# Optimization experiments

Measured on AMD Instinct MI355X. Metric: run time of the kernel, lower is better.

The kernel has to match this reference:

```python
import jax, jax.numpy as jnp
import numpy as np
import math

B, S, D_MODEL, H, D_K = 8, 1024, 512, 8, 64


def setup_inputs() -> dict:
    key = jax.random.key(0)
    ks = jax.random.split(key, 12)
    s = 1.0 / math.sqrt(D_MODEL)
    inp = {
        "q": jax.random.normal(ks[0], (B, S, D_MODEL), dtype=jnp.float32),
        "k": jax.random.normal(ks[1], (B, S, D_MODEL), dtype=jnp.float32),
        "v": jax.random.normal(ks[2], (B, S, D_MODEL), dtype=jnp.float32),
        "Wq": jax.random.normal(ks[3], (D_MODEL, D_MODEL), dtype=jnp.float32) * s,
        "bq": jnp.zeros((D_MODEL,), dtype=jnp.float32),
        "Wk": jax.random.normal(ks[4], (D_MODEL, D_MODEL), dtype=jnp.float32) * s,
        "bk": jnp.zeros((D_MODEL,), dtype=jnp.float32),
        "Wv": jax.random.normal(ks[5], (D_MODEL, D_MODEL), dtype=jnp.float32) * s,
        "bv": jnp.zeros((D_MODEL,), dtype=jnp.float32),
        "Wo": jax.random.normal(ks[6], (D_MODEL, D_MODEL), dtype=jnp.float32) * s,
        "bo": jnp.zeros((D_MODEL,), dtype=jnp.float32),
        # xavier_uniform on (H,1,1): bound = sqrt(6/(1+1)) ~ 1.732
        "gammas": jax.random.uniform(ks[7], (H, 1, 1), minval=-1.732, maxval=1.732, dtype=jnp.float32),
        "mask": jnp.triu(jnp.ones((S, S), dtype=bool), k=1),  # mask future positions
        "key_padding_mask": jnp.zeros((B, S), dtype=bool),
    }
    return inp


def reference(q, k, v, Wq, bq, Wk, bk, Wv, bv, Wo, bo, gammas, mask, key_padding_mask):
    bs, seqlen = q.shape[0], q.shape[1]
    NEG = -1e32

    def proj(x, W, b):
        # nn.Linear: x @ W.T + b, then split heads -> [b, h, s, d_k]
        return (x @ W.T + b).reshape(bs, seqlen, H, D_K).transpose(0, 2, 1, 3)

    qh, kh, vh = proj(q, Wq, bq), proj(k, Wk, bk), proj(v, Wv, bv)

    scores = jnp.einsum("bhqd,bhkd->bhqk", qh, kh) / math.sqrt(D_K)
    full_mask = mask[None, None, :, :] | key_padding_mask[:, None, None, :]  # [b,1,s,s] bcast over h

    # --- distance-decay branch (torch.no_grad / detach) ---
    scores_ = jax.nn.softmax(jnp.where(full_mask, NEG, scores), axis=-1)
    scores_ = scores_ * (~full_mask).astype(scores.dtype)
    distcum = jnp.cumsum(scores_, axis=-1)  # forward=True
    disttotal = jnp.sum(scores_, axis=-1, keepdims=True)
    idx = jnp.arange(seqlen)
    position_effect = jnp.abs(idx[None, :] - idx[:, None]).astype(scores.dtype)  # |i-j|
    dist_scores = jnp.sqrt(jnp.clip((disttotal - distcum) * position_effect, 0.0))
    dist_scores = jax.lax.stop_gradient(dist_scores)

    gamma = -jax.nn.softplus(gammas)[None]  # [1, h, 1, 1]
    total_effect = jnp.clip(jnp.exp(dist_scores * gamma), 1e-5, 1e5)

    attn = jax.nn.softmax(jnp.where(full_mask, NEG, scores * total_effect), axis=-1)
    out = jnp.einsum("bhqk,bhkd->bhqd", attn, vh)
    concat = out.transpose(0, 2, 1, 3).reshape(bs, seqlen, D_MODEL)
    return concat @ Wo.T + bo
```

## Files before the change

kernel.cpp:

```cpp
#include <hip/hip_runtime.h>
#include <hip/hip_bf16.h>
#include <math.h>

#define NB   8
#define NS   1024
#define NDM  512
#define NH   8
#define NDK  64
#define NM   8192

typedef __attribute__((ext_vector_type(8))) short short8;
typedef __attribute__((ext_vector_type(4))) float f32x4;

__device__ __forceinline__ unsigned short f2b(float f) {
    __hip_bfloat16 h = __float2bfloat16(f);
    unsigned short u;
    __builtin_memcpy(&u, &h, 2);
    return u;
}
__device__ __forceinline__ float b2f(unsigned short u) {
    return __uint_as_float(((unsigned)u) << 16);
}
__device__ __forceinline__ float exp2_raw(float x) { float r; asm("v_exp_f32 %0, %1" : "=v"(r) : "v"(x)); return r; }
__device__ __forceinline__ float sqrt_raw(float x) { float r; asm("v_sqrt_f32 %0, %1" : "=v"(r) : "v"(x)); return r; }
__device__ __forceinline__ float rcp_raw(float x)  { float r; asm("v_rcp_f32 %0, %1" : "=v"(r) : "v"(x)); return r; }

template<int CTRL, int RM>
__device__ __forceinline__ float dpp_mov0(float x) {
    int m = __builtin_amdgcn_update_dpp(0, __float_as_int(x), CTRL, RM, 0xf, true);
    return __int_as_float(m);
}
__device__ __forceinline__ float wave_incl_scan(float x) {
    x += dpp_mov0<0x111, 0xf>(x);
    x += dpp_mov0<0x112, 0xf>(x);
    x += dpp_mov0<0x114, 0xf>(x);
    x += dpp_mov0<0x118, 0xf>(x);
    x += dpp_mov0<0x142, 0xa>(x);
    x += dpp_mov0<0x143, 0xc>(x);
    return x;
}
__device__ __forceinline__ float lane63(float x) {
    return __int_as_float(__builtin_amdgcn_readlane(__float_as_int(x), 63));
}

__device__ __forceinline__ short8 pack8(float4 a, float4 b) {
    short8 r;
    r[0] = (short)f2b(a.x); r[1] = (short)f2b(a.y);
    r[2] = (short)f2b(a.z); r[3] = (short)f2b(a.w);
    r[4] = (short)f2b(b.x); r[5] = (short)f2b(b.y);
    r[6] = (short)f2b(b.z); r[7] = (short)f2b(b.w);
    return r;
}

template<int OMODE, bool ACVT>
__device__ __forceinline__ void gemm_body(unsigned short* As, unsigned short* Bs,
                                          const void* __restrict__ Ap,
                                          const float* __restrict__ Wf,
                                          const float* __restrict__ bias,
                                          void* __restrict__ outp) {
    const int tid  = threadIdx.x;
    const int lane = tid & 63;
    const int wid  = tid >> 6;
    const int l15  = lane & 15, lhi = lane >> 4;
    const int m0 = (blockIdx.x >> 2) * 128;
    const int n0 = (blockIdx.x & 3) * 128;
    const int wr = wid >> 1, wc = wid & 1;

    const float* Af = (const float*)Ap;
    const unsigned short* Ab = (const unsigned short*)Ap;

    f32x4 acc[4][4];
#pragma unroll
    for (int i = 0; i < 4; ++i)
#pragma unroll
        for (int j = 0; j < 4; ++j) acc[i][j] = (f32x4){0.f, 0.f, 0.f, 0.f};

    for (int kk0 = 0; kk0 < NDM; kk0 += 32) {
#pragma unroll
        for (int c = 0; c < 2; ++c) {
            int ci  = tid + 256 * c;
            int row = ci >> 2;
            int kc  = (ci & 3) << 3;
            short8 aval;
            if (ACVT) {
                const float* p = Af + (size_t)(m0 + row) * NDM + kk0 + kc;
                aval = pack8(*(const float4*)p, *(const float4*)(p + 4));
            } else {
                aval = *(const short8*)(Ab + (size_t)(m0 + row) * NDM + kk0 + kc);
            }
            *(short8*)(As + ci * 8) = aval;
            const float* qp = Wf + (size_t)(n0 + row) * NDM + kk0 + kc;
            *(short8*)(Bs + ci * 8) = pack8(*(const float4*)qp, *(const float4*)(qp + 4));
        }
        __syncthreads();
        short8 af[4], bf[4];
#pragma unroll
        for (int mi = 0; mi < 4; ++mi)
            af[mi] = *(const short8*)(As + (wr * 64 + mi * 16 + l15) * 32 + lhi * 8);
#pragma unroll
        for (int ni = 0; ni < 4; ++ni)
            bf[ni] = *(const short8*)(Bs + (wc * 64 + ni * 16 + l15) * 32 + lhi * 8);
#pragma unroll
        for (int mi = 0; mi < 4; ++mi)
#pragma unroll
            for (int ni = 0; ni < 4; ++ni)
                acc[mi][ni] = __builtin_amdgcn_mfma_f32_16x16x32_bf16(af[mi], bf[ni], acc[mi][ni], 0, 0, 0);
        __syncthreads();
    }

#pragma unroll
    for (int mi = 0; mi < 4; ++mi) {
#pragma unroll
        for (int ni = 0; ni < 4; ++ni) {
            int row0 = m0 + wr * 64 + mi * 16 + lhi * 4;
            int col  = n0 + wc * 64 + ni * 16 + l15;
            float bv = bias[col];
            if (OMODE == 0) {
                unsigned short* o = (unsigned short*)outp;
                int h = col >> 6, d = col & 63;
#pragma unroll
                for (int r = 0; r < 4; ++r) {
                    int m = row0 + r;
                    int b = m >> 10, s = m & 1023;
                    o[(size_t)(((b * NH + h) * NS) + s) * NDK + d] = f2b(acc[mi][ni][r] + bv);
                }
            } else if (OMODE == 1) {
                unsigned short* o = (unsigned short*)outp;
                int h = col >> 6, d = col & 63;
                int b = row0 >> 10, s0 = row0 & 1023;
                ushort4 u;
                u.x = f2b(acc[mi][ni][0] + bv);
                u.y = f2b(acc[mi][ni][1] + bv);
                u.z = f2b(acc[mi][ni][2] + bv);
                u.w = f2b(acc[mi][ni][3] + bv);
                *(ushort4*)(o + (size_t)((b * NH + h) * NDK + d) * NS + s0) = u;
            } else {
                float* o = (float*)outp;
#pragma unroll
                for (int r = 0; r < 4; ++r)
                    o[(size_t)(row0 + r) * NDM + col] = acc[mi][ni][r] + bv;
            }
        }
    }
}

__global__ __launch_bounds__(256) void qkv_gemm(const float* __restrict__ q,
                                                const float* __restrict__ k,
                                                const float* __restrict__ v,
                                                const float* __restrict__ Wq,
                                                const float* __restrict__ Wk,
                                                const float* __restrict__ Wv,
                                                const float* __restrict__ bq,
                                                const float* __restrict__ bk,
                                                const float* __restrict__ bv,
                                                unsigned short* __restrict__ Qh,
                                                unsigned short* __restrict__ Kh,
                                                unsigned short* __restrict__ Vt) {
    __shared__ unsigned short As[128 * 32];
    __shared__ unsigned short Bs[128 * 32];
    const int y = blockIdx.y;
    if (y == 0)      gemm_body<0, true>(As, Bs, q, Wq, bq, Qh);
    else if (y == 1) gemm_body<0, true>(As, Bs, k, Wk, bk, Kh);
    else             gemm_body<1, true>(As, Bs, v, Wv, bv, Vt);
}

__global__ __launch_bounds__(256) void wo_gemm(const unsigned short* __restrict__ A,
                                               const float* __restrict__ Wo,
                                               const float* __restrict__ bo,
                                               float* __restrict__ out) {
    __shared__ unsigned short As[128 * 32];
    __shared__ unsigned short Bs[128 * 32];
    gemm_body<2, false>(As, Bs, A, Wo, bo, out);
}

__global__ __launch_bounds__(256, 4) void attn_kernel(const unsigned short* __restrict__ Qh,
                                                      const unsigned short* __restrict__ Kh,
                                                      const unsigned short* __restrict__ Vt,
                                                      const float* __restrict__ gammas,
                                                      unsigned short* __restrict__ concat) {
    __shared__ unsigned short pb[16 * 1024];
    const int bh   = blockIdx.x & 63;
    const int pair = blockIdx.x >> 6;
    const int tid = threadIdx.x, lane = tid & 63, wid = tid >> 6;
    const int l15 = lane & 15, lhi = lane >> 4;
    const float SC = 0.125f * 1.44269504f;

    const unsigned short* Kb = Kh + (size_t)bh * NS * NDK;
    const unsigned short* Vb = Vt + (size_t)bh * NDK * NS;
    const float g  = gammas[bh & (NH - 1)];
    const float g2 = -log1pf(__expf(g)) * 1.44269504f;
    const int cb = lane * 16;
    const int bq_ = bh >> 3, hq = bh & 7;

    for (int hs = 0; hs < 2; ++hs) {
        const int qt = hs ? (63 - pair) : pair;
        const int r0 = qt * 16;
        const int C  = ((r0 + 16 + 63) >> 6) << 6;

        const unsigned short* Qb = Qh + (size_t)(bh * NS + r0) * NDK;
        short8 qf0 = *(const short8*)(Qb + l15 * NDK + lhi * 8);
        short8 qf1 = *(const short8*)(Qb + l15 * NDK + lhi * 8 + 32);
        for (int j0 = wid * 16; j0 < C; j0 += 64) {
            const unsigned short* kp = Kb + (size_t)(j0 + l15) * NDK + lhi * 8;
            short8 kf0 = *(const short8*)kp;
            short8 kf1 = *(const short8*)(kp + 32);
            f32x4 a = {0.f, 0.f, 0.f, 0.f};
            a = __builtin_amdgcn_mfma_f32_16x16x32_bf16(kf0, qf0, a, 0, 0, 0);
            a = __builtin_amdgcn_mfma_f32_16x16x32_bf16(kf1, qf1, a, 0, 0, 0);
            ushort4 u;
            u.x = f2b(a[0] * SC);
            u.y = f2b(a[1] * SC);
            u.z = f2b(a[2] * SC);
            u.w = f2b(a[3] * SC);
            int ch = ((j0 >> 3) + (lhi >> 1)) ^ l15;
            *(ushort4*)(pb + l15 * 1024 + ch * 8 + (lhi & 1) * 4) = u;
        }
        __syncthreads();

#pragma unroll
        for (int t = 0; t < 4; ++t) {
            const int rr = wid + 4 * t;
            const int i  = r0 + rr;
            unsigned short* rowp = pb + rr * 1024;
            short8 raw0 = *(const short8*)(rowp + (((2 * lane)     ^ rr) << 3));
            short8 raw1 = *(const short8*)(rowp + (((2 * lane + 1) ^ rr) << 3));
            float s[16];
#pragma unroll
            for (int u = 0; u < 8; ++u) {
                s[u]     = b2f((unsigned short)raw0[u]);
                s[8 + u] = b2f((unsigned short)raw1[u]);
            }
#pragma unroll
            for (int u = 0; u < 16; ++u)
                if (cb + u > i) s[u] = -1e30f;
            float p[16];
            float run = 0.f;
#pragma unroll
            for (int u = 0; u < 16; ++u) { run += exp2_raw(s[u]); p[u] = run; }
            const float inc      = wave_incl_scan(run);
            const float l1       = lane63(inc);
            const float invl1    = rcp_raw(l1);
            const float taillane = l1 - (inc - run);
            const float di       = (float)(i - cb);
            float l2 = 0.f;
#pragma unroll
            for (int u = 0; u < 16; ++u) {
                float tail = fmaxf(taillane - p[u], 0.f);
                float t2   = (tail * invl1) * (di - (float)u);
                float te   = fmaxf(exp2_raw(g2 * sqrt_raw(t2)), 1e-5f);
                float w    = exp2_raw(s[u] * te);
                s[u] = w;
                l2 += w;
            }
            const float l2t  = lane63(wave_incl_scan(l2));
            const float inv2 = rcp_raw(l2t);
            short8 h0, h1;
#pragma unroll
            for (int u = 0; u < 8; ++u) {
                h0[u] = (short)f2b(s[u] * inv2);
                h1[u] = (short)f2b(s[8 + u] * inv2);
            }
            *(short8*)(rowp + (((2 * lane)     ^ rr) << 3)) = h0;
            *(short8*)(rowp + (((2 * lane + 1) ^ rr) << 3)) = h1;
        }
        __syncthreads();

        const int d0 = wid * 16;
        f32x4 acc = {0.f, 0.f, 0.f, 0.f};
        for (int j0 = 0; j0 < C; j0 += 32) {
            short8 av = *(const short8*)(Vb + (size_t)(d0 + l15) * NS + j0 + lhi * 8);
            short8 pw = *(const short8*)(pb + l15 * 1024 + (((((j0 >> 3) + lhi)) ^ l15) << 3));
            acc = __builtin_amdgcn_mfma_f32_16x16x32_bf16(av, pw, acc, 0, 0, 0);
        }
        {
            int d = d0 + lhi * 4;
            int s = r0 + l15;
            ushort4 u;
            u.x = f2b(acc[0]); u.y = f2b(acc[1]);
            u.z = f2b(acc[2]); u.w = f2b(acc[3]);
            *(ushort4*)(concat + (size_t)(bq_ * NS + s) * NDM + hq * NDK + d) = u;
        }
        __syncthreads();
    }
}

extern "C" void kernel_launch(void* const* d_in, const int* in_sizes, int n_in,
                              void* d_out, int out_size, void* d_ws, size_t ws_size,
                              hipStream_t stream) {
    const float* q  = (const float*)d_in[0];
    const float* k  = (const float*)d_in[1];
    const float* v  = (const float*)d_in[2];
    const float* Wq = (const float*)d_in[3];
    const float* bq = (const float*)d_in[4];
    const float* Wk = (const float*)d_in[5];
    const float* bk = (const float*)d_in[6];
    const float* Wv = (const float*)d_in[7];
    const float* bv = (const float*)d_in[8];
    const float* Wo = (const float*)d_in[9];
    const float* bo = (const float*)d_in[10];
    const float* gm = (const float*)d_in[11];

    char* w = (char*)d_ws;
    unsigned short* Qh     = (unsigned short*)(w);
    unsigned short* Kh     = (unsigned short*)(w + (size_t)8388608);
    unsigned short* Vt     = (unsigned short*)(w + (size_t)16777216);
    unsigned short* concat = (unsigned short*)(w + (size_t)25165824);

    qkv_gemm<<<dim3(256, 3), dim3(256), 0, stream>>>(q, k, v, Wq, Wk, Wv, bq, bk, bv, Qh, Kh, Vt);
    attn_kernel<<<dim3(2048), dim3(256), 0, stream>>>(Qh, Kh, Vt, gm, concat);
    wo_gemm<<<dim3(256), dim3(256), 0, stream>>>(concat, Wo, bo, (float*)d_out);
}
```

Baseline: 135.7 us.

## Pre-convert QKV weights, retile GEMMs to 64x128 with swizzled LDS, halve attention row tiles

Adds a pre-pass that converts Wq/Wk/Wv to bf16 once, using the output buffer as scratch, so the QKV GEMM can stream B tiles with global_load_lds instead of converting fp32 inside every block. Both GEMMs move to 64x128 tiles with a K-step of 64 and an XOR-swizzled LDS layout, which doubles the grid and raises occupancy hints. The attention kernel splits each 16-row query tile into two 8-row halves across separate blocks, halving LDS use and doubling the block count for better occupancy. In exchange, half of each score MFMA's output and the final PV tile is discarded, so matrix-core work per useful row roughly doubles, and there is one extra launch.

```diff
diff --git a/kernel.cpp b/kernel.cpp
--- a/kernel.cpp
+++ b/kernel.cpp
@@ -52,67 +52,101 @@
     return r;
 }
 
-template<int OMODE, bool ACVT>
-__device__ __forceinline__ void gemm_body(unsigned short* As, unsigned short* Bs,
-                                          const void* __restrict__ Ap,
-                                          const float* __restrict__ Wf,
-                                          const float* __restrict__ bias,
-                                          void* __restrict__ outp) {
-    const int tid  = threadIdx.x;
-    const int lane = tid & 63;
-    const int wid  = tid >> 6;
-    const int l15  = lane & 15, lhi = lane >> 4;
-    const int m0 = (blockIdx.x >> 2) * 128;
+__device__ __forceinline__ void gload16(const unsigned short* g, unsigned short* l) {
+    __builtin_amdgcn_global_load_lds(
+        (const __attribute__((address_space(1))) void*)g,
+        (__attribute__((address_space(3))) void*)l, 16, 0, 0);
+}
+
+__global__ __launch_bounds__(256) void cvt_w3(const float* __restrict__ Wq,
+                                              const float* __restrict__ Wk,
+                                              const float* __restrict__ Wv,
+                                              unsigned short* __restrict__ out) {
+    int idx = blockIdx.x * 256 + threadIdx.x;
+    int m = idx >> 16;
+    const float* s = (m == 0) ? Wq : ((m == 1) ? Wk : Wv);
+    float4 f = *(const float4*)(s + (size_t)(idx & 65535) * 4);
+    ushort4 u;
+    u.x = f2b(f.x); u.y = f2b(f.y); u.z = f2b(f.z); u.w = f2b(f.w);
+    *(ushort4*)(out + (size_t)idx * 4) = u;
+}
+
+template<int OMODE, bool ACVT, bool BCVT>
+__device__ __forceinline__ void gemm_body64(unsigned short* As, unsigned short* Bs,
+                                            const void* __restrict__ Ap,
+                                            const void* __restrict__ Wp,
+                                            const float* __restrict__ bias,
+                                            void* __restrict__ outp) {
+    const int tid = threadIdx.x, lane = tid & 63, wid = tid >> 6;
+    const int l15 = lane & 15, lhi = lane >> 4;
+    const int m0 = (blockIdx.x >> 2) * 64;
     const int n0 = (blockIdx.x & 3) * 128;
     const int wr = wid >> 1, wc = wid & 1;
-
     const float* Af = (const float*)Ap;
     const unsigned short* Ab = (const unsigned short*)Ap;
-
-    f32x4 acc[4][4];
-#pragma unroll
-    for (int i = 0; i < 4; ++i)
+    const float* Wf = (const float*)Wp;
+    const unsigned short* Wb = (const unsigned short*)Wp;
+
+    f32x4 acc[2][4];
+#pragma unroll
+    for (int i = 0; i < 2; ++i)
 #pragma unroll
         for (int j = 0; j < 4; ++j) acc[i][j] = (f32x4){0.f, 0.f, 0.f, 0.f};
 
-    for (int kk0 = 0; kk0 < NDM; kk0 += 32) {
+    for (int kk0 = 0; kk0 < NDM; kk0 += 64) {
 #pragma unroll
         for (int c = 0; c < 2; ++c) {
-            int ci  = tid + 256 * c;
-            int row = ci >> 2;
-            int kc  = (ci & 3) << 3;
-            short8 aval;
+            int ci = tid + 256 * c, row = ci >> 3, ch = ci & 7;
+            int sch = ch ^ (row & 7);
             if (ACVT) {
-                const float* p = Af + (size_t)(m0 + row) * NDM + kk0 + kc;
-                aval = pack8(*(const float4*)p, *(const float4*)(p + 4));
+                const float* p = Af + (size_t)(m0 + row) * NDM + kk0 + ch * 8;
+                *(short8*)(As + row * 64 + sch * 8) = pack8(*(const float4*)p, *(const float4*)(p + 4));
             } else {
-                aval = *(const short8*)(Ab + (size_t)(m0 + row) * NDM + kk0 + kc);
-            }
-            *(short8*)(As + ci * 8) = aval;
-            const float* qp = Wf + (size_t)(n0 + row) * NDM + kk0 + kc;
-            *(short8*)(Bs + ci * 8) = pack8(*(const float4*)qp, *(const float4*)(qp + 4));
-        }
-        __syncthreads();
-        short8 af[4], bf[4];
-#pragma unroll
-        for (int mi = 0; mi < 4; ++mi)
-            af[mi] = *(const short8*)(As + (wr * 64 + mi * 16 + l15) * 32 + lhi * 8);
+                gload16(Ab + (size_t)(m0 + row) * NDM + kk0 + sch * 8, As + ci * 8);
+            }
+        }
+#pragma unroll
+        for (int c = 0; c < 4; ++c) {
+            int ci = tid + 256 * c, row = ci >> 3, ch = ci & 7;
+            int sch = ch ^ (row & 7);
+            if (BCVT) {
+                const float* p = Wf + (size_t)(n0 + row) * NDM + kk0 + ch * 8;
+                *(short8*)(Bs + row * 64 + sch * 8) = pack8(*(const float4*)p, *(const float4*)(p + 4));
+            } else {
+                gload16(Wb + (size_t)(n0 + row) * NDM + kk0 + sch * 8, Bs + ci * 8);
+            }
+        }
+        __syncthreads();
+        short8 af[2][2], bf[4][2];
+#pragma unroll
+        for (int mi = 0; mi < 2; ++mi)
+#pragma unroll
+            for (int kk = 0; kk < 2; ++kk) {
+                int row = wr * 32 + mi * 16 + l15;
+                af[mi][kk] = *(const short8*)(As + row * 64 + (((kk * 4 + lhi) ^ (l15 & 7)) << 3));
+            }
 #pragma unroll
         for (int ni = 0; ni < 4; ++ni)
-            bf[ni] = *(const short8*)(Bs + (wc * 64 + ni * 16 + l15) * 32 + lhi * 8);
-#pragma unroll
-        for (int mi = 0; mi < 4; ++mi)
-#pragma unroll
-            for (int ni = 0; ni < 4; ++ni)
-                acc[mi][ni] = __builtin_amdgcn_mfma_f32_16x16x32_bf16(af[mi], bf[ni], acc[mi][ni], 0, 0, 0);
+#pragma unroll
+            for (int kk = 0; kk < 2; ++kk) {
+                int row = wc * 64 + ni * 16 + l15;
+                bf[ni][kk] = *(const short8*)(Bs + row * 64 + (((kk * 4 + lhi) ^ (l15 & 7)) << 3));
+            }
+#pragma unroll
+        for (int mi = 0; mi < 2; ++mi)
+#pragma unroll
+            for (int ni = 0; ni < 4; ++ni) {
+                acc[mi][ni] = __builtin_amdgcn_mfma_f32_16x16x32_bf16(af[mi][0], bf[ni][0], acc[mi][ni], 0, 0, 0);
+                acc[mi][ni] = __builtin_amdgcn_mfma_f32_16x16x32_bf16(af[mi][1], bf[ni][1], acc[mi][ni], 0, 0, 0);
+            }
         __syncthreads();
     }
 
 #pragma unroll
-    for (int mi = 0; mi < 4; ++mi) {
+    for (int mi = 0; mi < 2; ++mi) {
 #pragma unroll
         for (int ni = 0; ni < 4; ++ni) {
-            int row0 = m0 + wr * 64 + mi * 16 + lhi * 4;
+            int row0 = m0 + wr * 32 + mi * 16 + lhi * 4;
             int col  = n0 + wc * 64 + ni * 16 + l15;
             float bv = bias[col];
             if (OMODE == 0) {
@@ -144,43 +178,45 @@
     }
 }
 
-__global__ __launch_bounds__(256) void qkv_gemm(const float* __restrict__ q,
-                                                const float* __restrict__ k,
-                                                const float* __restrict__ v,
-                                                const float* __restrict__ Wq,
-                                                const float* __restrict__ Wk,
-                                                const float* __restrict__ Wv,
-                                                const float* __restrict__ bq,
-                                                const float* __restrict__ bk,
-                                                const float* __restrict__ bv,
-                                                unsigned short* __restrict__ Qh,
-                                                unsigned short* __restrict__ Kh,
-                                                unsigned short* __restrict__ Vt) {
-    __shared__ unsigned short As[128 * 32];
-    __shared__ unsigned short Bs[128 * 32];
+__global__ __launch_bounds__(256, 4) void qkv_gemm(const float* __restrict__ q,
+                                                   const float* __restrict__ k,
+                                                   const float* __restrict__ v,
+                                                   const unsigned short* __restrict__ Wqb,
+                                                   const unsigned short* __restrict__ Wkb,
+                                                   const unsigned short* __restrict__ Wvb,
+                                                   const float* __restrict__ bq,
+                                                   const float* __restrict__ bk,
+                                                   const float* __restrict__ bv,
+                                                   unsigned short* __restrict__ Qh,
+                                                   unsigned short* __restrict__ Kh,
+                                                   unsigned short* __restrict__ Vt) {
+    __shared__ unsigned short As[64 * 64];
+    __shared__ unsigned short Bs[128 * 64];
     const int y = blockIdx.y;
-    if (y == 0)      gemm_body<0, true>(As, Bs, q, Wq, bq, Qh);
-    else if (y == 1) gemm_body<0, true>(As, Bs, k, Wk, bk, Kh);
-    else             gemm_body<1, true>(As, Bs, v, Wv, bv, Vt);
-}
-
-__global__ __launch_bounds__(256) void wo_gemm(const unsigned short* __restrict__ A,
-                                               const float* __restrict__ Wo,
-                                               const float* __restrict__ bo,
-                                               float* __restrict__ out) {
-    __shared__ unsigned short As[128 * 32];
-    __shared__ unsigned short Bs[128 * 32];
-    gemm_body<2, false>(As, Bs, A, Wo, bo, out);
-}
-
-__global__ __launch_bounds__(256, 4) void attn_kernel(const unsigned short* __restrict__ Qh,
+    if (y == 0)      gemm_body64<0, true, false>(As, Bs, q, Wqb, bq, Qh);
+    else if (y == 1) gemm_body64<0, true, false>(As, Bs, k, Wkb, bk, Kh);
+    else             gemm_body64<1, true, false>(As, Bs, v, Wvb, bv, Vt);
+}
+
+__global__ __launch_bounds__(256, 4) void wo_gemm(const unsigned short* __restrict__ A,
+                                                  const float* __restrict__ Wo,
+                                                  const float* __restrict__ bo,
+                                                  float* __restrict__ out) {
+    __shared__ unsigned short As[64 * 64];
+    __shared__ unsigned short Bs[128 * 64];
+    gemm_body64<2, false, true>(As, Bs, A, Wo, bo, out);
+}
+
+__global__ __launch_bounds__(256, 8) void attn_kernel(const unsigned short* __restrict__ Qh,
                                                       const unsigned short* __restrict__ Kh,
                                                       const unsigned short* __restrict__ Vt,
                                                       const float* __restrict__ gammas,
                                                       unsigned short* __restrict__ concat) {
-    __shared__ unsigned short pb[16 * 1024];
+    __shared__ unsigned short pb[8 * 1024];
     const int bh   = blockIdx.x & 63;
-    const int pair = blockIdx.x >> 6;
+    const int ph   = blockIdx.x >> 6;
+    const int half = ph & 1;
+    const int pair = ph >> 1;
     const int tid = threadIdx.x, lane = tid & 63, wid = tid >> 6;
     const int l15 = lane & 15, lhi = lane >> 4;
     const float SC = 0.125f * 1.44269504f;
@@ -193,11 +229,11 @@
     const int bq_ = bh >> 3, hq = bh & 7;
 
     for (int hs = 0; hs < 2; ++hs) {
-        const int qt = hs ? (63 - pair) : pair;
-        const int r0 = qt * 16;
-        const int C  = ((r0 + 16 + 63) >> 6) << 6;
-
-        const unsigned short* Qb = Qh + (size_t)(bh * NS + r0) * NDK;
+        const int qt  = hs ? (63 - pair) : pair;
+        const int r0h = qt * 16 + half * 8;
+        const int C   = ((r0h + 8 + 63) >> 6) << 6;
+
+        const unsigned short* Qb = Qh + (size_t)(bh * NS + qt * 16) * NDK;
         short8 qf0 = *(const short8*)(Qb + l15 * NDK + lhi * 8);
         short8 qf1 = *(const short8*)(Qb + l15 * NDK + lhi * 8 + 32);
         for (int j0 = wid * 16; j0 < C; j0 += 64) {
@@ -207,23 +243,26 @@
             f32x4 a = {0.f, 0.f, 0.f, 0.f};
             a = __builtin_amdgcn_mfma_f32_16x16x32_bf16(kf0, qf0, a, 0, 0, 0);
             a = __builtin_amdgcn_mfma_f32_16x16x32_bf16(kf1, qf1, a, 0, 0, 0);
-            ushort4 u;
-            u.x = f2b(a[0] * SC);
-            u.y = f2b(a[1] * SC);
-            u.z = f2b(a[2] * SC);
-            u.w = f2b(a[3] * SC);
-            int ch = ((j0 >> 3) + (lhi >> 1)) ^ l15;
-            *(ushort4*)(pb + l15 * 1024 + ch * 8 + (lhi & 1) * 4) = u;
-        }
-        __syncthreads();
-
-#pragma unroll
-        for (int t = 0; t < 4; ++t) {
-            const int rr = wid + 4 * t;
-            const int i  = r0 + rr;
-            unsigned short* rowp = pb + rr * 1024;
-            short8 raw0 = *(const short8*)(rowp + (((2 * lane)     ^ rr) << 3));
-            short8 raw1 = *(const short8*)(rowp + (((2 * lane + 1) ^ rr) << 3));
+            if ((l15 >> 3) == half) {
+                int rowl = l15 & 7;
+                ushort4 u;
+                u.x = f2b(a[0] * SC);
+                u.y = f2b(a[1] * SC);
+                u.z = f2b(a[2] * SC);
+                u.w = f2b(a[3] * SC);
+                int ch = (((j0 >> 3) + (lhi >> 1)) ^ rowl);
+                *(ushort4*)(pb + rowl * 1024 + ch * 8 + (lhi & 1) * 4) = u;
+            }
+        }
+        __syncthreads();
+
+#pragma unroll
+        for (int t = 0; t < 2; ++t) {
+            const int rrl = wid + 4 * t;
+            const int i   = r0h + rrl;
+            unsigned short* rowp = pb + rrl * 1024;
+            short8 raw0 = *(const short8*)(rowp + (((2 * lane)     ^ rrl) << 3));
+            short8 raw1 = *(const short8*)(rowp + (((2 * lane + 1) ^ rrl) << 3));
             float s[16];
 #pragma unroll
             for (int u = 0; u < 8; ++u) {
@@ -260,8 +299,8 @@
                 h0[u] = (short)f2b(s[u] * inv2);
                 h1[u] = (short)f2b(s[8 + u] * inv2);
             }
-            *(short8*)(rowp + (((2 * lane)     ^ rr) << 3)) = h0;
-            *(short8*)(rowp + (((2 * lane + 1) ^ rr) << 3)) = h1;
+            *(short8*)(rowp + (((2 * lane)     ^ rrl) << 3)) = h0;
+            *(short8*)(rowp + (((2 * lane + 1) ^ rrl) << 3)) = h1;
         }
         __syncthreads();
 
@@ -269,12 +308,13 @@
         f32x4 acc = {0.f, 0.f, 0.f, 0.f};
         for (int j0 = 0; j0 < C; j0 += 32) {
             short8 av = *(const short8*)(Vb + (size_t)(d0 + l15) * NS + j0 + lhi * 8);
-            short8 pw = *(const short8*)(pb + l15 * 1024 + (((((j0 >> 3) + lhi)) ^ l15) << 3));
+            int rowl = l15 & 7;
+            short8 pw = *(const short8*)(pb + rowl * 1024 + (((((j0 >> 3) + lhi)) ^ rowl) << 3));
             acc = __builtin_amdgcn_mfma_f32_16x16x32_bf16(av, pw, acc, 0, 0, 0);
         }
-        {
+        if (l15 < 8) {
             int d = d0 + lhi * 4;
-            int s = r0 + l15;
+            int s = r0h + l15;
             ushort4 u;
             u.x = f2b(acc[0]); u.y = f2b(acc[1]);
             u.z = f2b(acc[2]); u.w = f2b(acc[3]);
@@ -306,7 +346,12 @@
     unsigned short* Vt     = (unsigned short*)(w + (size_t)16777216);
     unsigned short* concat = (unsigned short*)(w + (size_t)25165824);
 
-    qkv_gemm<<<dim3(256, 3), dim3(256), 0, stream>>>(q, k, v, Wq, Wk, Wv, bq, bk, bv, Qh, Kh, Vt);
-    attn_kernel<<<dim3(2048), dim3(256), 0, stream>>>(Qh, Kh, Vt, gm, concat);
-    wo_gemm<<<dim3(256), dim3(256), 0, stream>>>(concat, Wo, bo, (float*)d_out);
-}
+    unsigned short* Wqb = (unsigned short*)d_out;
+    unsigned short* Wkb = Wqb + 262144;
+    unsigned short* Wvb = Wqb + 524288;
+
+    cvt_w3<<<dim3(768), dim3(256), 0, stream>>>(Wq, Wk, Wv, Wqb);
+    qkv_gemm<<<dim3(512, 3), dim3(256), 0, stream>>>(q, k, v, Wqb, Wkb, Wvb, bq, bk, bv, Qh, Kh, Vt);
+    attn_kernel<<<dim3(4096), dim3(256), 0, stream>>>(Qh, Kh, Vt, gm, concat);
+    wo_gemm<<<dim3(512), dim3(256), 0, stream>>>(concat, Wo, bo, (float*)d_out);
+}
```

After: 199.9 us. +47.3%, slower.
